# Optimization experiments

Measured on AMD Instinct MI355X. Metric: run time of the kernel, lower is better.

Reference implementation:

```python
import jax, jax.numpy as jnp
import numpy as np

NOISE_VAR = 0.001  # std of directional noise (torch Normal(0, noise_var) uses scale)
EPS_NORM = 1e-12
EPS_LOG = 1e-10


def setup_inputs() -> dict:
    key = jax.random.key(0)
    k1, k2, k3 = jax.random.split(key, 3)
    N, D, K = 32768, 256, 8192
    z = jax.random.normal(k1, (N, D), dtype=jnp.float32)
    # torch init: uniform * (1/num_embeddings)
    codebook = jax.random.uniform(k2, (K, D), dtype=jnp.float32) * (1.0 / K)
    noise = jax.random.normal(k3, (N, D), dtype=jnp.float32)
    return {"z": z, "codebook": codebook, "noise": noise}


def reference(z, codebook, noise):
    K = codebook.shape[0]
    # squared L2 distances via ||z||^2 + ||c||^2 - 2 z c^T   -> [N, K]
    distances = (jnp.sum(z * z, axis=1, keepdims=True)
                 + jnp.sum(codebook * codebook, axis=1)
                 - 2.0 * (z @ codebook.T))
    indices = jnp.argmin(distances, axis=1)              # [N]
    z_hard = codebook[indices]                           # [N, D] gather
    direction = z_hard - z
    random_vectors = noise * NOISE_VAR + direction
    norm_rv = jnp.linalg.norm(random_vectors, axis=1, keepdims=True)
    normalized = random_vectors / jnp.maximum(norm_rv, EPS_NORM)
    error_magnitude = jnp.linalg.norm(direction, axis=1, keepdims=True)
    vq_error = error_magnitude * jax.lax.stop_gradient(normalized)
    z_q = z + vq_error
    # perplexity
    counts = jnp.bincount(indices, length=K)
    avg_probs = counts.astype(jnp.float32) / indices.shape[0]
    perplexity = jnp.exp(-jnp.sum(avg_probs * jnp.log(avg_probs + EPS_LOG)))
    return z_q, indices, perplexity
```

## Files before the change

### kernel.cpp

```cpp
#include <hip/hip_runtime.h>
#include <math.h>

#define N_ROWS 32768
#define K_CODES 8192
#define D_DIM 256
#define GUARD_STEPS 4u
#define NCHUNK 256

typedef unsigned short u16;
typedef unsigned int u32;
typedef float f32x4 __attribute__((ext_vector_type(4)));
typedef short short8 __attribute__((ext_vector_type(8)));

#define GL_LDS(g, l) __builtin_amdgcn_global_load_lds( \
    (const __attribute__((address_space(1))) void*)(g), \
    (__attribute__((address_space(3))) void*)(l), 16, 0, 0)

__device__ __forceinline__ void bf16_split(float x, u16& h, u16& l) {
    unsigned u = __float_as_uint(x);
    unsigned r = (u + 0x7fffu + ((u >> 16) & 1u)) >> 16;
    h = (u16)r;
    float hf = __uint_as_float(r << 16);
    float res = x - hf;
    unsigned u2 = __float_as_uint(res);
    unsigned r2 = (u2 + 0x7fffu + ((u2 >> 16) & 1u)) >> 16;
    l = (u16)r2;
}

__global__ void split_norm_kernel(const float* __restrict__ x, u16* __restrict__ hi,
                                  u16* __restrict__ lo, float* __restrict__ nrm, int nrows) {
    int gid = blockIdx.x * blockDim.x + threadIdx.x;
    int row = gid >> 6;
    int lane = gid & 63;
    if (row >= nrows) return;
    float4 v = ((const float4*)(x + (size_t)row * D_DIM))[lane];
    ushort4 h, l;
    bf16_split(v.x, h.x, l.x);
    bf16_split(v.y, h.y, l.y);
    bf16_split(v.z, h.z, l.z);
    bf16_split(v.w, h.w, l.w);
    ((ushort4*)(hi + (size_t)row * D_DIM))[lane] = h;
    ((ushort4*)(lo + (size_t)row * D_DIM))[lane] = l;
    double s = (double)v.x * v.x + (double)v.y * v.y + (double)v.z * v.z + (double)v.w * v.w;
    #pragma unroll
    for (int off = 32; off; off >>= 1) s += __shfl_xor(s, off);
    if (lane == 0) nrm[row] = (float)s;
}

__global__ void row_norms_kernel(const float* __restrict__ x, float* __restrict__ nrm, int nrows) {
    int gid = blockIdx.x * blockDim.x + threadIdx.x;
    int row = gid >> 6;
    int lane = gid & 63;
    if (row >= nrows) return;
    float4 v = ((const float4*)(x + (size_t)row * D_DIM))[lane];
    double s = (double)v.x * v.x + (double)v.y * v.y + (double)v.z * v.z + (double)v.w * v.w;
    #pragma unroll
    for (int off = 32; off; off >>= 1) s += __shfl_xor(s, off);
    if (lane == 0) nrm[row] = (float)s;
}

__global__ __launch_bounds__(512, 2) void mfma_pass_kernel(
    const u16* __restrict__ z1, const u16* __restrict__ z2,
    const u16* __restrict__ c1, const u16* __restrict__ c2,
    const float* __restrict__ rowN,
    int* __restrict__ idx_i, float* __restrict__ idx_f, int* __restrict__ cand2,
    int* __restrict__ flag_list, int* __restrict__ flag_count)
{
    __shared__ __align__(16) u16 z1s[32 * 128 * 8];
    __shared__ __align__(16) u16 z2s[2][4 * 128 * 8];
    __shared__ __align__(16) u16 c1s[2][4 * 256 * 8];
    __shared__ __align__(16) u16 c2s[2][4 * 256 * 8];

    const int tid = threadIdx.x;
    const int lane = tid & 63;
    const int w = tid >> 6;
    const int wm = w >> 2, wn = w & 3;
    const int l15 = lane & 15, l4 = lane >> 4;
    const int row0 = blockIdx.x * 128;

    #pragma unroll
    for (int r = 0; r < 8; ++r) {
        int s = tid + 512 * r;
        int seg = s >> 7, rw = s & 127;
        GL_LDS(z1 + (size_t)(row0 + rw) * D_DIM + seg * 8, z1s + s * 8);
    }

    auto stage_chunk = [&](int c, int buf) {
        const int ct = c >> 3, kc = c & 7;
        const int cb = ct * 256, ko = kc * 32;
        {
            int seg = tid >> 7, rw = tid & 127;
            GL_LDS(z2 + (size_t)(row0 + rw) * D_DIM + ko + seg * 8, z2s[buf] + tid * 8);
        }
        #pragma unroll
        for (int r = 0; r < 2; ++r) {
            int s = tid + 512 * r;
            int seg = s >> 8, cr = s & 255;
            GL_LDS(c1 + (size_t)(cb + cr) * D_DIM + ko + seg * 8, c1s[buf] + s * 8);
        }
        #pragma unroll
        for (int r = 0; r < 2; ++r) {
            int s = tid + 512 * r;
            int seg = s >> 8, cr = s & 255;
            GL_LDS(c2 + (size_t)(cb + cr) * D_DIM + ko + seg * 8, c2s[buf] + s * 8);
        }
    };

    float rnv[16];
    u32 rnb[16];
    #pragma unroll
    for (int fm = 0; fm < 4; ++fm)
        #pragma unroll
        for (int r = 0; r < 4; ++r) {
            float rv = rowN[row0 + wm * 64 + fm * 16 + l4 * 4 + r];
            rnv[fm * 4 + r] = rv;
            rnb[fm * 4 + r] = __float_as_uint(rv) - 1024u;
        }

    u32 b1k[16], b2k[16];
    #pragma unroll
    for (int k = 0; k < 16; ++k) { b1k[k] = 0xFFFFFFFFu; b2k[k] = 0xFFFFFFFFu; }

    f32x4 acc[4][4];
    #pragma unroll
    for (int fm = 0; fm < 4; ++fm)
        #pragma unroll
        for (int fn = 0; fn < 4; ++fn) acc[fm][fn] = (f32x4){0.f, 0.f, 0.f, 0.f};

    stage_chunk(0, 0);

    for (int c = 0; c < NCHUNK; ++c) {
        const int buf = c & 1;
        const int kc = c & 7;

        if (c + 1 < NCHUNK) {
            stage_chunk(c + 1, buf ^ 1);
            asm volatile("s_waitcnt vmcnt(5)" ::: "memory");
        } else {
            asm volatile("s_waitcnt vmcnt(0)" ::: "memory");
        }
        __builtin_amdgcn_s_barrier();

        short8 a1[4], a2[4], b1f[4], b2f[4];
        #pragma unroll
        for (int fm = 0; fm < 4; ++fm) {
            int rw = wm * 64 + fm * 16 + l15;
            a1[fm] = *(const short8*)(z1s + ((kc * 4 + l4) * 128 + rw) * 8);
            a2[fm] = *(const short8*)(z2s[buf] + (l4 * 128 + rw) * 8);
        }
        #pragma unroll
        for (int fn = 0; fn < 4; ++fn) {
            int cr = wn * 64 + fn * 16 + l15;
            b1f[fn] = *(const short8*)(c1s[buf] + (l4 * 256 + cr) * 8);
            b2f[fn] = *(const short8*)(c2s[buf] + (l4 * 256 + cr) * 8);
        }

        asm volatile("s_waitcnt lgkmcnt(0)" ::: "memory");
        __builtin_amdgcn_sched_barrier(0);
        __builtin_amdgcn_s_setprio(1);
        #pragma unroll
        for (int fm = 0; fm < 4; ++fm)
            #pragma unroll
            for (int fn = 0; fn < 4; ++fn) {
                acc[fm][fn] = __builtin_amdgcn_mfma_f32_16x16x32_bf16(a1[fm], b1f[fn], acc[fm][fn], 0, 0, 0);
                acc[fm][fn] = __builtin_amdgcn_mfma_f32_16x16x32_bf16(a2[fm], b1f[fn], acc[fm][fn], 0, 0, 0);
                acc[fm][fn] = __builtin_amdgcn_mfma_f32_16x16x32_bf16(a1[fm], b2f[fn], acc[fm][fn], 0, 0, 0);
            }
        __builtin_amdgcn_s_setprio(0);
        __builtin_amdgcn_s_barrier();

        if (kc == 7) {
            const int cbase = (c >> 3) * 256;
            #pragma unroll
            for (int fn = 0; fn < 4; ++fn) {
                u32 code = (u32)(cbase + wn * 64 + fn * 16 + l15);
                #pragma unroll
                for (int fm = 0; fm < 4; ++fm)
                    #pragma unroll
                    for (int r2 = 0; r2 < 4; ++r2) {
                        int k16 = fm * 4 + r2;
                        float dist = fmaf(-2.0f, acc[fm][fn][r2], rnv[k16]);
                        u32 key = ((__float_as_uint(dist) - rnb[k16]) << 13) + code;
                        u32 mx = b1k[k16] > key ? b1k[k16] : key;
                        b1k[k16] = b1k[k16] < key ? b1k[k16] : key;
                        b2k[k16] = b2k[k16] < mx ? b2k[k16] : mx;
                        acc[fm][fn][r2] = 0.f;
                    }
            }
        }
    }

    #pragma unroll
    for (int off = 1; off < 16; off <<= 1) {
        #pragma unroll
        for (int k = 0; k < 16; ++k) {
            u32 o1 = (u32)__shfl_xor((int)b1k[k], off);
            u32 o2 = (u32)__shfl_xor((int)b2k[k], off);
            u32 mx = b1k[k] > o1 ? b1k[k] : o1;
            b1k[k] = b1k[k] < o1 ? b1k[k] : o1;
            u32 mn2 = b2k[k] < o2 ? b2k[k] : o2;
            b2k[k] = mn2 < mx ? mn2 : mx;
        }
    }
    __syncthreads();
    u32* mk1 = (u32*)&z2s[0][0];
    u32* mk2 = mk1 + 512;
    if (l15 == 0) {
        #pragma unroll
        for (int fm = 0; fm < 4; ++fm)
            #pragma unroll
            for (int r2 = 0; r2 < 4; ++r2) {
                int rl = wm * 64 + fm * 16 + l4 * 4 + r2;
                mk1[wn * 128 + rl] = b1k[fm * 4 + r2];
                mk2[wn * 128 + rl] = b2k[fm * 4 + r2];
            }
    }
    __syncthreads();
    if (tid < 128) {
        u32 B1 = 0xFFFFFFFFu, B2 = 0xFFFFFFFFu;
        #pragma unroll
        for (int s = 0; s < 4; ++s) {
            u32 o1 = mk1[s * 128 + tid];
            u32 o2 = mk2[s * 128 + tid];
            u32 mx = B1 > o1 ? B1 : o1;
            B1 = B1 < o1 ? B1 : o1;
            u32 mn2 = B2 < o2 ? B2 : o2;
            B2 = mn2 < mx ? mn2 : mx;
        }
        int row = row0 + tid;
        int i1 = (int)(B1 & 8191u);
        idx_i[row] = i1;
        idx_f[row] = (float)i1;
        cand2[row] = (int)(B2 & 8191u);
        if ((B2 >> 13) - (B1 >> 13) <= GUARD_STEPS) {
            int p = atomicAdd(flag_count, 1);
            flag_list[p] = row;
        }
    }
}

__global__ __launch_bounds__(256) void lite_rescan_kernel(
    const float* __restrict__ z, const float* __restrict__ cb,
    const float* __restrict__ rowN, const int* __restrict__ flag_list,
    const int* __restrict__ flag_count, const int* __restrict__ cand2,
    int* __restrict__ idx_i, float* __restrict__ idx_f)
{
    int nflag = *flag_count;
    int widx = blockIdx.x * 4 + (threadIdx.x >> 6);
    if (widx >= nflag) return;
    int lane = threadIdx.x & 63;
    int row = flag_list[widx];
    int i1 = idx_i[row];
    int i2 = cand2[row];
    float rn = rowN[row];
    float4 zv = *(const float4*)(z + (size_t)row * D_DIM + lane * 4);
    float4 c1v = *(const float4*)(cb + (size_t)i1 * D_DIM + lane * 4);
    float4 c2v = *(const float4*)(cb + (size_t)i2 * D_DIM + lane * 4);
    float s1 = zv.x * c1v.x;
    s1 = fmaf(zv.y, c1v.y, s1);
    s1 = fmaf(zv.z, c1v.z, s1);
    s1 = fmaf(zv.w, c1v.w, s1);
    float s2 = zv.x * c2v.x;
    s2 = fmaf(zv.y, c2v.y, s2);
    s2 = fmaf(zv.z, c2v.z, s2);
    s2 = fmaf(zv.w, c2v.w, s2);
    #pragma unroll
    for (int off = 32; off; off >>= 1) {
        s1 += __shfl_xor(s1, off);
        s2 += __shfl_xor(s2, off);
    }
    float d1 = fmaf(-2.0f, s1, rn);
    float d2 = fmaf(-2.0f, s2, rn);
    bool w2 = (d2 < d1) || (d2 == d1 && i2 < i1);
    int win = w2 ? i2 : i1;
    if (lane == 0) {
        idx_i[row] = win;
        idx_f[row] = (float)win;
    }
}

__global__ void finalize_kernel(const float* __restrict__ z, const float* __restrict__ cb,
                                const float* __restrict__ noise, const int* __restrict__ idx,
                                float* __restrict__ zq)
{
    int gid = blockIdx.x * blockDim.x + threadIdx.x;
    int row = gid >> 6;
    int lane = gid & 63;
    if (row >= N_ROWS) return;
    const float4* zr = (const float4*)(z + (size_t)row * D_DIM);
    const float4* nr = (const float4*)(noise + (size_t)row * D_DIM);
    int k = idx[row];
    const float4* cr = (const float4*)(cb + (size_t)k * D_DIM);
    float4 zv = zr[lane], nv = nr[lane], cv = cr[lane];
    float4 dir, rv;
    dir.x = cv.x - zv.x; dir.y = cv.y - zv.y; dir.z = cv.z - zv.z; dir.w = cv.w - zv.w;
    rv.x = nv.x * 0.001f + dir.x; rv.y = nv.y * 0.001f + dir.y;
    rv.z = nv.z * 0.001f + dir.z; rv.w = nv.w * 0.001f + dir.w;
    float s_d = dir.x*dir.x + dir.y*dir.y + dir.z*dir.z + dir.w*dir.w;
    float s_r = rv.x*rv.x + rv.y*rv.y + rv.z*rv.z + rv.w*rv.w;
    #pragma unroll
    for (int off = 32; off; off >>= 1) {
        s_d += __shfl_xor(s_d, off);
        s_r += __shfl_xor(s_r, off);
    }
    float mag = sqrtf(s_d);
    float nrm = sqrtf(s_r);
    float scale = mag / fmaxf(nrm, 1e-12f);
    float4 o;
    o.x = zv.x + rv.x * scale; o.y = zv.y + rv.y * scale;
    o.z = zv.z + rv.z * scale; o.w = zv.w + rv.w * scale;
    ((float4*)(zq + (size_t)row * D_DIM))[lane] = o;
}

__global__ void zero_kernel(int* __restrict__ h, int* __restrict__ cnt) {
    int i = blockIdx.x * 256 + threadIdx.x;
    if (i < K_CODES) h[i] = 0;
    if (i == K_CODES) *cnt = 0;
}
__global__ void hist_kernel(const int* __restrict__ idx, int* __restrict__ h) {
    int i = blockIdx.x * blockDim.x + threadIdx.x;
    if (i < N_ROWS) atomicAdd(&h[idx[i]], 1);
}
__global__ void perplexity_kernel(const int* __restrict__ h, float* __restrict__ out) {
    __shared__ double red[256];
    int tid = threadIdx.x;
    double s = 0.0;
    for (int j = tid; j < K_CODES; j += 256) {
        float p = (float)h[j] / 32768.0f;
        float t = p * logf(p + 1e-10f);
        s += (double)t;
    }
    red[tid] = s;
    __syncthreads();
    for (int off = 128; off; off >>= 1) {
        if (tid < off) red[tid] += red[tid + off];
        __syncthreads();
    }
    if (tid == 0) out[0] = (float)exp(-red[0]);
}

#define BM 64
#define BN 128
#define BD 32
#define TM 4
#define TN 8
__global__ __launch_bounds__(256) void argmin_kernel(
    const float* __restrict__ z, const float* __restrict__ cb,
    const float* __restrict__ rowN, const float* __restrict__ codeN,
    int* __restrict__ idx_out, float* __restrict__ idx_f_out)
{
    __shared__ float As[BD][BM + 4];
    __shared__ float Bs[BD][BN + 4];
    const int tid = threadIdx.x;
    const int tx = tid & 15;
    const int ty = tid >> 4;
    const int row0 = blockIdx.x * BM;
    float rn[TM];
    #pragma unroll
    for (int tm = 0; tm < TM; ++tm) rn[tm] = rowN[row0 + ty * TM + tm];
    float bestVal[TM]; int bestIdx[TM];
    #pragma unroll
    for (int tm = 0; tm < TM; ++tm) { bestVal[tm] = INFINITY; bestIdx[tm] = 0; }
    for (int t0 = 0; t0 < K_CODES; t0 += BN) {
        float acc[TM][TN];
        #pragma unroll
        for (int tm = 0; tm < TM; ++tm)
            #pragma unroll
            for (int tn = 0; tn < TN; ++tn) acc[tm][tn] = 0.0f;
        for (int d0 = 0; d0 < D_DIM; d0 += BD) {
            __syncthreads();
            #pragma unroll
            for (int r = 0; r < 2; ++r) {
                int g = tid + 256 * r;
                int m = g >> 3, seg = g & 7;
                float4 v = *(const float4*)(z + (size_t)(row0 + m) * D_DIM + d0 + seg * 4);
                As[seg * 4 + 0][m] = v.x; As[seg * 4 + 1][m] = v.y;
                As[seg * 4 + 2][m] = v.z; As[seg * 4 + 3][m] = v.w;
            }
            #pragma unroll
            for (int r = 0; r < 4; ++r) {
                int g = tid + 256 * r;
                int c = g >> 3, seg = g & 7;
                float4 v = *(const float4*)(cb + (size_t)(t0 + c) * D_DIM + d0 + seg * 4);
                Bs[seg * 4 + 0][c] = v.x; Bs[seg * 4 + 1][c] = v.y;
                Bs[seg * 4 + 2][c] = v.z; Bs[seg * 4 + 3][c] = v.w;
            }
            __syncthreads();
            #pragma unroll
            for (int d = 0; d < BD; ++d) {
                float a[TM], b[TN];
                #pragma unroll
                for (int tm = 0; tm < TM; ++tm) a[tm] = As[d][ty * TM + tm];
                #pragma unroll
                for (int tn = 0; tn < TN; ++tn) b[tn] = Bs[d][tx * TN + tn];
                #pragma unroll
                for (int tm = 0; tm < TM; ++tm)
                    #pragma unroll
                    for (int tn = 0; tn < TN; ++tn)
                        acc[tm][tn] = fmaf(a[tm], b[tn], acc[tm][tn]);
            }
        }
        #pragma unroll
        for (int tn = 0; tn < TN; ++tn) {
            int code = t0 + tx * TN + tn;
            float cn = codeN[code];
            #pragma unroll
            for (int tm = 0; tm < TM; ++tm) {
                float c2 = 2.0f * acc[tm][tn];
                float ts = rn[tm] + cn;
                float dist = ts - c2;
                if (dist < bestVal[tm]) { bestVal[tm] = dist; bestIdx[tm] = code; }
            }
        }
    }
    #pragma unroll
    for (int off = 8; off; off >>= 1) {
        #pragma unroll
        for (int tm = 0; tm < TM; ++tm) {
            float ov = __shfl_xor(bestVal[tm], off, 16);
            int   oi = __shfl_xor(bestIdx[tm], off, 16);
            if (ov < bestVal[tm] || (ov == bestVal[tm] && oi < bestIdx[tm])) {
                bestVal[tm] = ov; bestIdx[tm] = oi;
            }
        }
    }
    if (tx == 0) {
        #pragma unroll
        for (int tm = 0; tm < TM; ++tm) {
            int row = row0 + ty * TM + tm;
            idx_out[row] = bestIdx[tm];
            idx_f_out[row] = (float)bestIdx[tm];
        }
    }
}

extern "C" void kernel_launch(void* const* d_in, const int* in_sizes, int n_in,
                              void* d_out, int out_size, void* d_ws, size_t ws_size,
                              hipStream_t stream)
{
    const float* z     = (const float*)d_in[0];
    const float* cb    = (const float*)d_in[1];
    const float* noise = (const float*)d_in[2];

    float* out   = (float*)d_out;
    float* zq    = out;
    float* idx_f = out + (size_t)N_ROWS * D_DIM;
    float* perp  = idx_f + N_ROWS;

    char* ws = (char*)d_ws;

    const size_t OFF_Z1    = 0;
    const size_t OFF_Z2    = 16777216;
    const size_t OFF_C1    = 33554432;
    const size_t OFF_C2    = 37748736;
    const size_t OFF_ROWN  = 41943040;
    const size_t OFF_CODN  = 42074112;
    const size_t OFF_IDX   = 42106880;
    const size_t OFF_FLAGL = 42237952;
    const size_t OFF_FLAGC = 42369024;
    const size_t OFF_HIST  = 42369280;
    const size_t OFF_CAND2 = 42402048;
    const size_t NEED      = 42533120;

    if (ws_size >= NEED) {
        u16*   z1    = (u16*)(ws + OFF_Z1);
        u16*   z2    = (u16*)(ws + OFF_Z2);
        u16*   c1    = (u16*)(ws + OFF_C1);
        u16*   c2    = (u16*)(ws + OFF_C2);
        float* rowN  = (float*)(ws + OFF_ROWN);
        int*   idxi  = (int*)(ws + OFF_IDX);
        int*   flagl = (int*)(ws + OFF_FLAGL);
        int*   flagc = (int*)(ws + OFF_FLAGC);
        int*   hist  = (int*)(ws + OFF_HIST);
        int*   cand2 = (int*)(ws + OFF_CAND2);

        split_norm_kernel<<<N_ROWS / 4, 256, 0, stream>>>(z, z1, z2, rowN, N_ROWS);
        split_norm_kernel<<<K_CODES / 4, 256, 0, stream>>>(cb, c1, c2, (float*)(ws + OFF_CODN), K_CODES);
        zero_kernel<<<33, 256, 0, stream>>>(hist, flagc);
        mfma_pass_kernel<<<N_ROWS / 128, 512, 0, stream>>>(z1, z2, c1, c2, rowN,
                                                           idxi, idx_f, cand2, flagl, flagc);
        lite_rescan_kernel<<<N_ROWS / 4, 256, 0, stream>>>(z, cb, rowN, flagl, flagc,
                                                           cand2, idxi, idx_f);
        hist_kernel<<<N_ROWS / 256, 256, 0, stream>>>(idxi, hist);
        finalize_kernel<<<(N_ROWS * 64) / 256, 256, 0, stream>>>(z, cb, noise, idxi, zq);
        perplexity_kernel<<<1, 256, 0, stream>>>(hist, perp);
    } else {
        int*   idxi  = (int*)ws;
        int*   hist  = (int*)(ws + (size_t)N_ROWS * 4);
        float* rowN  = (float*)(ws + (size_t)(N_ROWS + K_CODES) * 4);
        float* codeN = (float*)(ws + (size_t)(2 * N_ROWS + K_CODES) * 4);
        int*   fc    = (int*)(ws + (size_t)(2 * N_ROWS + 2 * K_CODES) * 4);

        row_norms_kernel<<<N_ROWS / 4, 256, 0, stream>>>(z, rowN, N_ROWS);
        row_norms_kernel<<<K_CODES / 4, 256, 0, stream>>>(cb, codeN, K_CODES);
        argmin_kernel<<<N_ROWS / BM, 256, 0, stream>>>(z, cb, rowN, codeN, idxi, idx_f);
        zero_kernel<<<33, 256, 0, stream>>>(hist, fc);
        hist_kernel<<<N_ROWS / 256, 256, 0, stream>>>(idxi, hist);
        finalize_kernel<<<(N_ROWS * 64) / 256, 256, 0, stream>>>(z, cb, noise, idxi, zq);
        perplexity_kernel<<<1, 256, 0, stream>>>(hist, perp);
    }
}
```

Measured before the change: 638.7 us.

## Triple-buffer LDS staging with two-chunk-ahead prefetch and one barrier per chunk

Replaces the resident full-K z1 tile and double-buffered chunks with a three-deep ring of per-chunk buffers for z1, z2, c1 and c2. Loads are issued two chunks ahead, after the fragment reads, so the global-to-LDS copies overlap the MFMA work, and each iteration needs only one barrier. The MFMA order is regrouped into three passes and the priority and sched barriers are removed. z1 is now re-fetched for every chunk rather than loaded once, adding global traffic, and LDS use changes, which may affect occupancy.

```diff
diff --git a/kernel.cpp b/kernel.cpp
--- a/kernel.cpp
+++ b/kernel.cpp
@@ -66,10 +66,10 @@
     int* __restrict__ idx_i, float* __restrict__ idx_f, int* __restrict__ cand2,
     int* __restrict__ flag_list, int* __restrict__ flag_count)
 {
-    __shared__ __align__(16) u16 z1s[32 * 128 * 8];
-    __shared__ __align__(16) u16 z2s[2][4 * 128 * 8];
-    __shared__ __align__(16) u16 c1s[2][4 * 256 * 8];
-    __shared__ __align__(16) u16 c2s[2][4 * 256 * 8];
+    __shared__ __align__(16) u16 z1s[3][512 * 8];
+    __shared__ __align__(16) u16 z2s[3][512 * 8];
+    __shared__ __align__(16) u16 c1s[3][1024 * 8];
+    __shared__ __align__(16) u16 c2s[3][1024 * 8];
 
     const int tid = threadIdx.x;
     const int lane = tid & 63;
@@ -78,18 +78,12 @@
     const int l15 = lane & 15, l4 = lane >> 4;
     const int row0 = blockIdx.x * 128;
 
-    #pragma unroll
-    for (int r = 0; r < 8; ++r) {
-        int s = tid + 512 * r;
-        int seg = s >> 7, rw = s & 127;
-        GL_LDS(z1 + (size_t)(row0 + rw) * D_DIM + seg * 8, z1s + s * 8);
-    }
-
     auto stage_chunk = [&](int c, int buf) {
         const int ct = c >> 3, kc = c & 7;
         const int cb = ct * 256, ko = kc * 32;
         {
             int seg = tid >> 7, rw = tid & 127;
+            GL_LDS(z1 + (size_t)(row0 + rw) * D_DIM + ko + seg * 8, z1s[buf] + tid * 8);
             GL_LDS(z2 + (size_t)(row0 + rw) * D_DIM + ko + seg * 8, z2s[buf] + tid * 8);
         }
         #pragma unroll
@@ -97,11 +91,6 @@
             int s = tid + 512 * r;
             int seg = s >> 8, cr = s & 255;
             GL_LDS(c1 + (size_t)(cb + cr) * D_DIM + ko + seg * 8, c1s[buf] + s * 8);
-        }
-        #pragma unroll
-        for (int r = 0; r < 2; ++r) {
-            int s = tid + 512 * r;
-            int seg = s >> 8, cr = s & 255;
             GL_LDS(c2 + (size_t)(cb + cr) * D_DIM + ko + seg * 8, c2s[buf] + s * 8);
         }
     };
@@ -116,6 +105,7 @@
             rnv[fm * 4 + r] = rv;
             rnb[fm * 4 + r] = __float_as_uint(rv) - 1024u;
         }
+    asm volatile("s_waitcnt vmcnt(0)" ::: "memory");
 
     u32 b1k[16], b2k[16];
     #pragma unroll
@@ -128,45 +118,53 @@
         for (int fn = 0; fn < 4; ++fn) acc[fm][fn] = (f32x4){0.f, 0.f, 0.f, 0.f};
 
     stage_chunk(0, 0);
-
+    stage_chunk(1, 1);
+    asm volatile("s_waitcnt vmcnt(6)" ::: "memory");
+    __builtin_amdgcn_s_barrier();
+
+    int rb = 0;
     for (int c = 0; c < NCHUNK; ++c) {
-        const int buf = c & 1;
         const int kc = c & 7;
-
-        if (c + 1 < NCHUNK) {
-            stage_chunk(c + 1, buf ^ 1);
-            asm volatile("s_waitcnt vmcnt(5)" ::: "memory");
-        } else {
-            asm volatile("s_waitcnt vmcnt(0)" ::: "memory");
-        }
-        __builtin_amdgcn_s_barrier();
+        asm volatile("" ::: "memory");
 
         short8 a1[4], a2[4], b1f[4], b2f[4];
         #pragma unroll
         for (int fm = 0; fm < 4; ++fm) {
             int rw = wm * 64 + fm * 16 + l15;
-            a1[fm] = *(const short8*)(z1s + ((kc * 4 + l4) * 128 + rw) * 8);
-            a2[fm] = *(const short8*)(z2s[buf] + (l4 * 128 + rw) * 8);
+            a1[fm] = *(const short8*)(z1s[rb] + (l4 * 128 + rw) * 8);
+            a2[fm] = *(const short8*)(z2s[rb] + (l4 * 128 + rw) * 8);
         }
         #pragma unroll
         for (int fn = 0; fn < 4; ++fn) {
             int cr = wn * 64 + fn * 16 + l15;
-            b1f[fn] = *(const short8*)(c1s[buf] + (l4 * 256 + cr) * 8);
-            b2f[fn] = *(const short8*)(c2s[buf] + (l4 * 256 + cr) * 8);
-        }
-
+            b1f[fn] = *(const short8*)(c1s[rb] + (l4 * 256 + cr) * 8);
+            b2f[fn] = *(const short8*)(c2s[rb] + (l4 * 256 + cr) * 8);
+        }
+
+        if (c + 2 < NCHUNK) {
+            int sb = rb + 2; if (sb >= 3) sb -= 3;
+            stage_chunk(c + 2, sb);
+        }
+
+        #pragma unroll
+        for (int fm = 0; fm < 4; ++fm)
+            #pragma unroll
+            for (int fn = 0; fn < 4; ++fn)
+                acc[fm][fn] = __builtin_amdgcn_mfma_f32_16x16x32_bf16(a1[fm], b1f[fn], acc[fm][fn], 0, 0, 0);
+        #pragma unroll
+        for (int fm = 0; fm < 4; ++fm)
+            #pragma unroll
+            for (int fn = 0; fn < 4; ++fn)
+                acc[fm][fn] = __builtin_amdgcn_mfma_f32_16x16x32_bf16(a2[fm], b1f[fn], acc[fm][fn], 0, 0, 0);
+        #pragma unroll
+        for (int fm = 0; fm < 4; ++fm)
+            #pragma unroll
+            for (int fn = 0; fn < 4; ++fn)
+                acc[fm][fn] = __builtin_amdgcn_mfma_f32_16x16x32_bf16(a1[fm], b2f[fn], acc[fm][fn], 0, 0, 0);
+
+        if (c + 2 < NCHUNK) { asm volatile("s_waitcnt vmcnt(6)" ::: "memory"); }
+        else                { asm volatile("s_waitcnt vmcnt(0)" ::: "memory"); }
         asm volatile("s_waitcnt lgkmcnt(0)" ::: "memory");
-        __builtin_amdgcn_sched_barrier(0);
-        __builtin_amdgcn_s_setprio(1);
-        #pragma unroll
-        for (int fm = 0; fm < 4; ++fm)
-            #pragma unroll
-            for (int fn = 0; fn < 4; ++fn) {
-                acc[fm][fn] = __builtin_amdgcn_mfma_f32_16x16x32_bf16(a1[fm], b1f[fn], acc[fm][fn], 0, 0, 0);
-                acc[fm][fn] = __builtin_amdgcn_mfma_f32_16x16x32_bf16(a2[fm], b1f[fn], acc[fm][fn], 0, 0, 0);
-                acc[fm][fn] = __builtin_amdgcn_mfma_f32_16x16x32_bf16(a1[fm], b2f[fn], acc[fm][fn], 0, 0, 0);
-            }
-        __builtin_amdgcn_s_setprio(0);
         __builtin_amdgcn_s_barrier();
 
         if (kc == 7) {
@@ -188,6 +186,7 @@
                     }
             }
         }
+        rb = rb + 1; if (rb >= 3) rb -= 3;
     }
 
     #pragma unroll
@@ -203,7 +202,7 @@
         }
     }
     __syncthreads();
-    u32* mk1 = (u32*)&z2s[0][0];
+    u32* mk1 = (u32*)&z1s[0][0];
     u32* mk2 = mk1 + 512;
     if (l15 == 0) {
         #pragma unroll
```

Result: slower. 718.7 us (+12.5%).
